# Kernel optimization log

Hardware: AMD Instinct MI355X
Metric: run time of the kernel (lower is better)

## Reference

```python
import jax, jax.numpy as jnp
import numpy as np


def _cosine_alpha_bar(T, s=0.008):
    x = np.linspace(0.0, T, T + 1)
    ac = np.cos((x / T + s) / (1.0 + s) * np.pi / 2.0) ** 2
    ac = ac / ac[0]
    betas = np.clip(1.0 - ac[1:] / ac[:-1], 1e-5, 0.999)
    return jnp.asarray(np.cumprod(1.0 - betas), dtype=jnp.float32)


def setup_inputs():
    B, T, C, D, L, NS = 16, 1024, 16, 256, 4, 1000
    ks = list(jax.random.split(jax.random.key(0), 64))
    def w(i, shape, fan):
        return jax.random.normal(ks[i], shape, dtype=jnp.float32) / np.sqrt(fan)
    half = D // 2
    nf = half // 2
    inp = {}
    inp['x'] = jax.random.normal(ks[0], (B, T, C), dtype=jnp.float32)
    inp['t'] = jax.random.randint(ks[1], (B,), 0, NS, dtype=jnp.int32)
    dt = jax.random.uniform(ks[2], (B, T), minval=5e-4, maxval=2e-3, dtype=jnp.float32)
    inp['timestamps'] = jnp.cumsum(dt, axis=1)
    inp['mask'] = (jax.random.uniform(ks[3], (B, T, C)) > 0.3).astype(jnp.float32)
    inp['noise'] = jax.random.normal(ks[4], (B, T, D), dtype=jnp.float32)
    inp['n_heads'] = 4
    inp['alpha_bar'] = _cosine_alpha_bar(NS)
    inp['W_enc'] = w(5, (2 * C, D), 2 * C); inp['b_enc'] = jnp.zeros((D,), jnp.float32)
    inp['te_freqs'] = jnp.exp(-jnp.arange(half, dtype=jnp.float32) * np.log(10000.0) / half)
    inp['W_temb'] = w(6, (D, D), D); inp['b_temb'] = jnp.zeros((D,), jnp.float32)
    inp['th_a'] = 0.1 * jax.random.normal(ks[7], (half,), dtype=jnp.float32)
    inp['th_b'] = 0.1 * jax.random.normal(ks[8], (half,), dtype=jnp.float32)
    inp['th_freqs'] = (jnp.exp(-jnp.linspace(0.0, np.log(10000.0 / 4.0), nf)) * (2.0 * np.pi / 4.0)).astype(jnp.float32)
    inp['W_film'] = w(9, (D, 2 * D), D); inp['b_film'] = jnp.zeros((2 * D,), jnp.float32)
    inp['gru_Wih'] = w(10, (D, 3 * D), D); inp['gru_Whh'] = w(11, (D, 3 * D), D)
    inp['gru_bih'] = jnp.zeros((3 * D,), jnp.float32); inp['gru_bhh'] = jnp.zeros((3 * D,), jnp.float32)
    inp['ode_W1'] = w(12, (D, D), D); inp['ode_b1'] = jnp.zeros((D,), jnp.float32)
    inp['ode_W2'] = w(13, (D, D), D); inp['ode_b2'] = jnp.zeros((D,), jnp.float32)
    inp['tr_Wqkv'] = w(14, (L, D, 3 * D), D); inp['tr_bqkv'] = jnp.zeros((L, 3 * D), jnp.float32)
    inp['tr_Wo'] = w(15, (L, D, D), D); inp['tr_bo'] = jnp.zeros((L, D), jnp.float32)
    inp['tr_ln1_w'] = jnp.ones((L, D), jnp.float32); inp['tr_ln1_b'] = jnp.zeros((L, D), jnp.float32)
    inp['tr_ln2_w'] = jnp.ones((L, D), jnp.float32); inp['tr_ln2_b'] = jnp.zeros((L, D), jnp.float32)
    inp['tr_W1'] = w(16, (L, D, 4 * D), D); inp['tr_b1'] = jnp.zeros((L, 4 * D), jnp.float32)
    inp['tr_W2'] = w(17, (L, 4 * D, D), 4 * D); inp['tr_b2'] = jnp.zeros((L, D), jnp.float32)
    inp['trn_w'] = jnp.ones((D,), jnp.float32); inp['trn_b'] = jnp.zeros((D,), jnp.float32)
    return inp


def _ln(u, w_, b_):
    m = u.mean(-1, keepdims=True)
    v = u.var(-1, keepdims=True)
    return (u - m) / jnp.sqrt(v + 1e-5) * w_ + b_


def reference(x, t, timestamps, mask, noise, n_heads, alpha_bar, W_enc, b_enc, te_freqs, W_temb, b_temb, th_a, th_b, th_freqs, W_film, b_film, gru_Wih, gru_Whh, gru_bih, gru_bhh, ode_W1, ode_b1, ode_W2, ode_b2, tr_Wqkv, tr_bqkv, tr_Wo, tr_bo, tr_ln1_w, tr_ln1_b, tr_ln2_w, tr_ln2_b, tr_W1, tr_b1, tr_W2, tr_b2, trn_w, trn_b):
    B, T, C = x.shape
    D = W_enc.shape[1]
    hd = D // n_heads
    # latent encode + forward diffusion
    z = jax.nn.relu(jnp.concatenate([x, mask], -1) @ W_enc + b_enc)  # (B,T,D)
    ab = alpha_bar[t][:, None, None]
    h = jnp.sqrt(ab) * z + jnp.sqrt(1.0 - ab) * noise
    # diffusion-step sinusoidal embedding
    targ = t.astype(jnp.float32)[:, None] * te_freqs[None, :]
    te = (jnp.concatenate([jnp.sin(targ), jnp.cos(targ)], -1) @ W_temb + b_temb)[:, None, :]
    # TimeHybridEncoding: odd dims ramp, even dims interleaved sin/cos
    ts = timestamps
    ramp = ts[..., None] * th_a + th_b                       # (B,T,D/2)
    phase = ts[..., None] * th_freqs                         # (B,T,D/4)
    sc = jnp.stack([jnp.sin(phase), jnp.cos(phase)], -1).reshape(B, T, -1)
    tm = jnp.zeros((B, T, D), x.dtype).at[..., 0::2].set(sc).at[..., 1::2].set(ramp)
    gamma, beta = jnp.split(jax.nn.silu(te) @ W_film + b_film, 2, -1)
    tm = (1.0 + gamma) * tm + beta
    h = h + te + tm
    # Jump-ODE encoder: RK4 between events + GRUCell jump, as a scan
    dts = jnp.concatenate([jnp.zeros((B, 1), x.dtype), ts[:, 1:] - ts[:, :-1]], 1)[..., None]  # (B,T,1); dt0=0 -> identity ODE step
    def odef(hh):
        return jnp.tanh(hh @ ode_W1 + ode_b1) @ ode_W2 + ode_b2
    def step(hh, inp):
        xt, dt = inp
        f1 = odef(hh)
        f2 = odef(hh + 0.5 * dt * f1)
        f3 = odef(hh + 0.5 * dt * f2)
        f4 = odef(hh + dt * f3)
        hh = hh + dt / 6.0 * (f1 + 2.0 * f2 + 2.0 * f3 + f4)
        gi = xt @ gru_Wih + gru_bih
        gh = hh @ gru_Whh + gru_bhh
        ir, iz, inn = jnp.split(gi, 3, -1)
        hr, hz, hn = jnp.split(gh, 3, -1)
        r = jax.nn.sigmoid(ir + hr)
        zg = jax.nn.sigmoid(iz + hz)
        n = jnp.tanh(inn + r * hn)
        hh = (1.0 - zg) * n + zg * hh
        return hh, hh
    _, Hs = jax.lax.scan(step, jnp.zeros((B, D), x.dtype), (jnp.swapaxes(h, 0, 1), jnp.swapaxes(dts, 0, 1)))
    Hseq = jnp.swapaxes(Hs, 0, 1)  # (B,T,D)
    # pre-norm causal transformer encoder (eval mode, relu FFN), final LayerNorm
    causal = jnp.triu(jnp.full((T, T), -jnp.inf, dtype=x.dtype), 1)
    Ht = Hseq
    for l in range(tr_Wqkv.shape[0]):
        u = _ln(Ht, tr_ln1_w[l], tr_ln1_b[l])
        q, k, v = jnp.split(u @ tr_Wqkv[l] + tr_bqkv[l], 3, -1)
        q = q.reshape(B, T, n_heads, hd).transpose(0, 2, 1, 3)
        k = k.reshape(B, T, n_heads, hd).transpose(0, 2, 1, 3)
        v = v.reshape(B, T, n_heads, hd).transpose(0, 2, 1, 3)
        att = jax.nn.softmax(jnp.einsum('bhqd,bhkd->bhqk', q, k) / np.sqrt(hd) + causal, axis=-1)
        o = jnp.einsum('bhqk,bhkd->bhqd', att, v).transpose(0, 2, 1, 3).reshape(B, T, D)
        Ht = Ht + o @ tr_Wo[l] + tr_bo[l]
        u2 = _ln(Ht, tr_ln2_w[l], tr_ln2_b[l])
        Ht = Ht + jax.nn.relu(u2 @ tr_W1[l] + tr_b1[l]) @ tr_W2[l] + tr_b2[l]
    Ht = _ln(Ht, trn_w, trn_b)
    return Hseq + Ht
```

## Files before the change

### kernel.cpp

```cpp
#include <hip/hip_runtime.h>

#define Bz  16
#define Tz  1024
#define Cz  16
#define Dz  256
#define NHz 4
#define HDz 64
#define Lz  4
#define MROWS (Bz*Tz)
#define QB  8

__device__ __forceinline__ float sigmoidf_(float x){ return 1.0f/(1.0f+__expf(-x)); }
__device__ __forceinline__ float tanh_(float x){
  float e = __expf(2.f*x);
  return 1.f - 2.f/(e + 1.f);
}

__device__ __forceinline__ float dot2f(uint a, uint b, float c){
  float d;
  asm("v_dot2_f32_f16 %0, %1, %2, %3" : "=v"(d) : "v"(a), "v"(b), "v"(c));
  return d;
}
__device__ __forceinline__ uint f2h2(float a, float b){
  union { _Float16 h[2]; uint u; } r;
  r.h[0] = (_Float16)a; r.h[1] = (_Float16)b;
  return r.u;
}

__device__ __forceinline__ float red8(float a){
  int x = __builtin_amdgcn_update_dpp(0, __float_as_int(a), 0xB1, 0xF, 0xF, true);
  a += __int_as_float(x);
  x = __builtin_amdgcn_update_dpp(0, __float_as_int(a), 0x4E, 0xF, 0xF, true);
  a += __int_as_float(x);
  a += __shfl_xor(a, 4);
  return a;
}

#define BARSYNC() do{ \
  asm volatile("s_waitcnt lgkmcnt(0)" ::: "memory"); \
  __builtin_amdgcn_s_barrier(); \
}while(0)

typedef const __attribute__((address_space(1))) void* as1p;
typedef __attribute__((address_space(3))) void* as3p;

__global__ __launch_bounds__(256) void k_prep(
    const float* __restrict__ W1, const float* __restrict__ W2, const float* __restrict__ Whh,
    const float* __restrict__ bih, const float* __restrict__ bhh,
    uint* __restrict__ W1L, uint* __restrict__ W2L, uint* __restrict__ WhL,
    float* __restrict__ biasC)
{
  int m = blockIdx.x*256 + threadIdx.x;
  if (m < 65536){
    const float* W = (m < 32768) ? W1 : W2;
    uint* out = (m < 32768) ? W1L : W2L;
    int mm = m & 32767;
    int q = mm >> 2, cc = mm & 3;
    int i = q >> 9, l = q & 511;
    int j4 = l >> 3, ks = l & 7;
    int kp = ks*16 + i;
    int c = j4*4 + cc;
    out[mm] = f2h2(W[(2*kp)*256 + c], W[(2*kp+1)*256 + c]);
  } else if (m < 65536 + 98304){
    int mm = m - 65536;
    int g = mm >> 15;
    int r = mm & 32767;
    int q = r >> 2, cc = r & 3;
    int i = q >> 9, l = q & 511;
    int j4 = l >> 3, ks = l & 7;
    int kp = ks*16 + i;
    int c = j4*4 + cc;
    WhL[mm] = f2h2(Whh[(2*kp)*768 + g*256 + c], Whh[(2*kp+1)*768 + g*256 + c]);
  } else if (m < 65536 + 98304 + 768){
    int c = m - (65536 + 98304);
    biasC[c] = bih[c] + ((c < 512) ? bhh[c] : 0.f);
  }
}

__global__ __launch_bounds__(256) void k_batch_emb(
    const int* __restrict__ t, const float* __restrict__ te_freqs,
    const float* __restrict__ W_temb, const float* __restrict__ b_temb,
    const float* __restrict__ W_film, const float* __restrict__ b_film,
    float* __restrict__ te_out, float* __restrict__ gamma_out, float* __restrict__ beta_out)
{
  int b = blockIdx.x; int j = threadIdx.x;
  __shared__ float s[256];
  __shared__ float ste[256];
  float tf = (float)t[b];
  if (j < 128){
    float targ = tf * te_freqs[j];
    s[j]     = __sinf(targ);
    s[j+128] = __cosf(targ);
  }
  __syncthreads();
  float a0=0,a1=0,a2=0,a3=0;
  #pragma unroll 8
  for (int k=0;k<256;k+=4){
    a0 = fmaf(s[k+0], W_temb[(k+0)*256+j], a0);
    a1 = fmaf(s[k+1], W_temb[(k+1)*256+j], a1);
    a2 = fmaf(s[k+2], W_temb[(k+2)*256+j], a2);
    a3 = fmaf(s[k+3], W_temb[(k+3)*256+j], a3);
  }
  float te = (a0+a1)+(a2+a3) + b_temb[j];
  te_out[b*256+j] = te;
  ste[j] = te * sigmoidf_(te);
  __syncthreads();
  float g0=0,g1=0,h0=0,h1=0;
  #pragma unroll 8
  for (int k=0;k<256;k+=2){
    float v0 = ste[k+0], v1 = ste[k+1];
    g0 = fmaf(v0, W_film[(k+0)*512+j],     g0);
    g1 = fmaf(v1, W_film[(k+1)*512+j],     g1);
    h0 = fmaf(v0, W_film[(k+0)*512+256+j], h0);
    h1 = fmaf(v1, W_film[(k+1)*512+256+j], h1);
  }
  gamma_out[b*256+j] = g0+g1 + b_film[j];
  beta_out [b*256+j] = h0+h1 + b_film[256+j];
}

__global__ __launch_bounds__(256) void k_encode(
    const float* __restrict__ x, const float* __restrict__ mask, const float* __restrict__ noise,
    const int* __restrict__ t, const float* __restrict__ alpha_bar, const float* __restrict__ ts,
    const float* __restrict__ W_enc, const float* __restrict__ b_enc,
    const float* __restrict__ th_a, const float* __restrict__ th_b, const float* __restrict__ th_freqs,
    const float* __restrict__ te, const float* __restrict__ gamma, const float* __restrict__ beta,
    float* __restrict__ H0)
{
  int bt = blockIdx.x; int b = bt >> 10;
  int j = threadIdx.x;
  __shared__ float in[32];
  if (j < 16)      in[j] = x[bt*16 + j];
  else if (j < 32) in[j] = mask[bt*16 + (j-16)];
  __syncthreads();
  float acc = 0.f;
  #pragma unroll
  for (int k=0;k<32;k++) acc = fmaf(in[k], W_enc[k*256+j], acc);
  float z = fmaxf(acc + b_enc[j], 0.f);
  float ab = alpha_bar[t[b]];
  float h = sqrtf(ab)*z + sqrtf(1.f-ab)*noise[(size_t)bt*256 + j];
  float tsv = ts[bt];
  float tm;
  if (j & 1){
    int i = (j-1) >> 1;
    tm = fmaf(tsv, th_a[i], th_b[i]);
  } else {
    int m = j >> 2;
    float ph = tsv * th_freqs[m];
    tm = ((j & 3) == 0) ? __sinf(ph) : __cosf(ph);
  }
  tm = fmaf(1.f + gamma[b*256+j], tm, beta[b*256+j]);
  H0[(size_t)bt*256 + j] = h + te[b*256+j] + tm;
}

template<bool RELU, bool RES>
__global__ __launch_bounds__(256) void k_gemm(
    const float* __restrict__ A, const float* __restrict__ W,
    const float* __restrict__ bias, const float* __restrict__ Rp,
    float* __restrict__ Cp, int M, int N, int K)
{
  __shared__ float As[16][68];
  __shared__ float Bs[16][64];
  int bn = blockIdx.x * 64, bm = blockIdx.y * 64;
  int tid = threadIdx.x;
  int tx = tid & 15, ty = tid >> 4;
  float acc[4][4] = {};
  for (int k0=0; k0<K; k0+=16){
    #pragma unroll
    for (int i=0;i<4;i++){
      int idx = tid + i*256;
      int m = idx >> 4, kk = idx & 15;
      As[kk][m] = A[(size_t)(bm+m)*K + k0+kk];
    }
    #pragma unroll
    for (int i=0;i<4;i++){
      int idx = tid + i*256;
      int kk = idx >> 6, n = idx & 63;
      Bs[kk][n] = W[(size_t)(k0+kk)*N + bn+n];
    }
    __syncthreads();
    #pragma unroll
    for (int kk=0;kk<16;kk++){
      float a0=As[kk][ty*4+0], a1=As[kk][ty*4+1], a2=As[kk][ty*4+2], a3=As[kk][ty*4+3];
      float b0=Bs[kk][tx*4+0], b1=Bs[kk][tx*4+1], b2=Bs[kk][tx*4+2], b3=Bs[kk][tx*4+3];
      acc[0][0]=fmaf(a0,b0,acc[0][0]); acc[0][1]=fmaf(a0,b1,acc[0][1]); acc[0][2]=fmaf(a0,b2,acc[0][2]); acc[0][3]=fmaf(a0,b3,acc[0][3]);
      acc[1][0]=fmaf(a1,b0,acc[1][0]); acc[1][1]=fmaf(a1,b1,acc[1][1]); acc[1][2]=fmaf(a1,b2,acc[1][2]); acc[1][3]=fmaf(a1,b3,acc[1][3]);
      acc[2][0]=fmaf(a2,b0,acc[2][0]); acc[2][1]=fmaf(a2,b1,acc[2][1]); acc[2][2]=fmaf(a2,b2,acc[2][2]); acc[2][3]=fmaf(a2,b3,acc[2][3]);
      acc[3][0]=fmaf(a3,b0,acc[3][0]); acc[3][1]=fmaf(a3,b1,acc[3][1]); acc[3][2]=fmaf(a3,b2,acc[3][2]); acc[3][3]=fmaf(a3,b3,acc[3][3]);
    }
    __syncthreads();
  }
  #pragma unroll
  for (int i=0;i<4;i++){
    int row = bm + ty*4 + i;
    #pragma unroll
    for (int jj=0;jj<4;jj++){
      int col = bn + tx*4 + jj;
      float v = acc[i][jj] + bias[col];
      if (RELU) v = fmaxf(v, 0.f);
      if (RES)  v += Rp[(size_t)row*N + col];
      Cp[(size_t)row*N + col] = v;
    }
  }
}

#define W1_BYTES   131072
#define RING_OFF   131072
#define RING_BYTES 24576
#define V2_OFF     (RING_OFF + RING_BYTES)
#define SCAN_LDS_BYTES (V2_OFF + 1280)

#define DOT4V(WV, VW) { uint4 _w = (WV); \
  a0 = dot2f(_w.x, VW, a0); a1 = dot2f(_w.y, VW, a1); \
  a2 = dot2f(_w.z, VW, a2); a3 = dot2f(_w.w, VW, a3); }

#define MV16L(VB) { \
  uint4 q0=(VB)[ks5+0], q1=(VB)[ks5+1], q2=(VB)[ks5+2], q3=(VB)[ks5+3]; \
  DOT4V(w1s[0*512+tid], q0.x)  DOT4V(w1s[1*512+tid], q0.y)  DOT4V(w1s[2*512+tid], q0.z)  DOT4V(w1s[3*512+tid], q0.w)  \
  DOT4V(w1s[4*512+tid], q1.x)  DOT4V(w1s[5*512+tid], q1.y)  DOT4V(w1s[6*512+tid], q1.z)  DOT4V(w1s[7*512+tid], q1.w)  \
  DOT4V(w1s[8*512+tid], q2.x)  DOT4V(w1s[9*512+tid], q2.y)  DOT4V(w1s[10*512+tid], q2.z) DOT4V(w1s[11*512+tid], q2.w) \
  DOT4V(w1s[12*512+tid], q3.x) DOT4V(w1s[13*512+tid], q3.y) DOT4V(w1s[14*512+tid], q3.z) DOT4V(w1s[15*512+tid], q3.w) }

#define MV16R(W, VB) { \
  uint4 q0=(VB)[ks5+0], q1=(VB)[ks5+1], q2=(VB)[ks5+2], q3=(VB)[ks5+3]; \
  DOT4V(W[0], q0.x)  DOT4V(W[1], q0.y)  DOT4V(W[2], q0.z)  DOT4V(W[3], q0.w)  \
  DOT4V(W[4], q1.x)  DOT4V(W[5], q1.y)  DOT4V(W[6], q1.z)  DOT4V(W[7], q1.w)  \
  DOT4V(W[8], q2.x)  DOT4V(W[9], q2.y)  DOT4V(W[10], q2.z) DOT4V(W[11], q2.w) \
  DOT4V(W[12], q3.x) DOT4V(W[13], q3.y) DOT4V(W[14], q3.z) DOT4V(W[15], q3.w) }

#define RING_STEP(S, N, G0,G1,G2,G3) { \
  asm volatile("s_waitcnt vmcnt(" #N ")" ::: "memory"); \
  uint4 wv = *(const uint4*)(ringRd + (((S)%3)<<10) + lane16); \
  G0 = dot2f(wv.x, vw[(S)&15], G0); G1 = dot2f(wv.y, vw[(S)&15], G1); \
  G2 = dot2f(wv.z, vw[(S)&15], G2); G3 = dot2f(wv.w, vw[(S)&15], G3); \
  __builtin_amdgcn_global_load_lds((as1p)(WhL4 + ((((S)+3)%48)<<9) + tid), \
                                   (as3p)(ringRd + (((S)%3)<<10)), 16, 0, 0); \
}

__global__ __launch_bounds__(512) void k_scan(
    const uint* __restrict__ W1Lg, const uint* __restrict__ W2Lg, const uint* __restrict__ WhLg,
    const float* __restrict__ GI, const float* __restrict__ ts,
    const float* __restrict__ b1, const float* __restrict__ b2,
    const float* __restrict__ bhh, float* __restrict__ Hseq)
{
  extern __shared__ __align__(16) char smem[];
  uint4* w1s = (uint4*)smem;
  uint*  v2  = (uint*)(smem + V2_OFF);
  const int b = blockIdx.x, tid = threadIdx.x;
  const int j4 = tid >> 3, ks = tid & 7;
  const int ks5 = ks*5;
  char* ringRd = smem + RING_OFF + (tid >> 6)*3072;
  const int lane16 = (tid & 63) << 4;
  const uint4* W1L4 = (const uint4*)W1Lg;
  const uint4* W2L4 = (const uint4*)W2Lg;
  const uint4* WhL4 = (const uint4*)WhLg;
  #pragma unroll
  for (int i=0;i<16;i++) w1s[i*512+tid] = W1L4[i*512+tid];
  uint4 w2r[16];
  #pragma unroll
  for (int i=0;i<16;i++) w2r[i] = W2L4[i*512 + tid];
  if (tid < 320) v2[tid] = 0u;
  const float4 b1v  = ((const float4*)b1)[j4];
  const float4 b2v  = ((const float4*)b2)[j4];
  const float4 bhnv = ((const float4*)bhh)[128 + j4];
  const float* tsb = ts + b*Tz;
  const float* gib = GI + (size_t)b*Tz*768;
  float* hsq = Hseq + (size_t)b*Tz*256;
  const int wdw = 2*j4;
  const int wslot = (wdw >> 4)*20 + (wdw & 15);
  float4 h = {0.f,0.f,0.f,0.f};
  int cur = 0;
  float tprev = 0.f;
  __syncthreads();

  #pragma unroll
  for (int s=0;s<3;s++)
    __builtin_amdgcn_global_load_lds((as1p)(WhL4 + (s<<9) + tid),
                                     (as3p)(ringRd + (s<<10)), 16, 0, 0);
  float4 gi_r = *(const float4*)(gib + 0*768       + j4*4);
  float4 gi_z = *(const float4*)(gib + 0*768 + 256 + j4*4);
  float4 gi_n = *(const float4*)(gib + 0*768 + 512 + j4*4);

  for (int tt=0; tt<Tz; ++tt){
    float tcur = tsb[tt];
    float dt = tcur - tprev; if (tt == 0) dt = 0.f;
    tprev = tcur;
    uint* bufA = v2 + (cur ? 160 : 0);
    uint* bufB = v2 + (cur ? 0 : 160);
    const uint4* vbA = (const uint4*)bufA;
    const uint4* vbB = (const uint4*)bufB;

    {
      float a0=0,a1=0,a2=0,a3=0;
      MV16L(vbA);
      a0=red8(a0); a1=red8(a1); a2=red8(a2); a3=red8(a3);
      float u0 = tanh_(a0+b1v.x), u1 = tanh_(a1+b1v.y);
      float u2 = tanh_(a2+b1v.z), u3 = tanh_(a3+b1v.w);
      if (ks == 0){
        uint2 pk; pk.x = f2h2(u0,u1); pk.y = f2h2(u2,u3);
        *(uint2*)(bufB + wslot) = pk;
      }
    }
    BARSYNC();
    float4 hn;
    {
      float a0=0,a1=0,a2=0,a3=0;
      MV16R(w2r, vbB);
      a0=red8(a0); a1=red8(a1); a2=red8(a2); a3=red8(a3);
      hn.x = fmaf(dt, a0+b2v.x, h.x);
      hn.y = fmaf(dt, a1+b2v.y, h.y);
      hn.z = fmaf(dt, a2+b2v.z, h.z);
      hn.w = fmaf(dt, a3+b2v.w, h.w);
      if (ks == 0){
        uint2 pk; pk.x = f2h2(hn.x,hn.y); pk.y = f2h2(hn.z,hn.w);
        *(uint2*)(bufA + wslot) = pk;
      }
    }
    BARSYNC();
    {
      uint4 q0=vbA[ks5+0], q1=vbA[ks5+1], q2=vbA[ks5+2], q3=vbA[ks5+3];
      uint vw[16] = {q0.x,q0.y,q0.z,q0.w, q1.x,q1.y,q1.z,q1.w,
                     q2.x,q2.y,q2.z,q2.w, q3.x,q3.y,q3.z,q3.w};
      float r0=0,r1=0,r2=0,r3=0, z0=0,z1=0,z2=0,z3=0, n0=0,n1=0,n2=0,n3=0;
      RING_STEP(0,3, r0,r1,r2,r3)  RING_STEP(1,3, r0,r1,r2,r3)
      RING_STEP(2,3, r0,r1,r2,r3)  RING_STEP(3,2, r0,r1,r2,r3)
      RING_STEP(4,2, r0,r1,r2,r3)  RING_STEP(5,2, r0,r1,r2,r3)
      RING_STEP(6,2, r0,r1,r2,r3)  RING_STEP(7,2, r0,r1,r2,r3)
      RING_STEP(8,2, r0,r1,r2,r3)  RING_STEP(9,2, r0,r1,r2,r3)
      RING_STEP(10,2, r0,r1,r2,r3) RING_STEP(11,2, r0,r1,r2,r3)
      RING_STEP(12,2, r0,r1,r2,r3) RING_STEP(13,2, r0,r1,r2,r3)
      RING_STEP(14,2, r0,r1,r2,r3) RING_STEP(15,2, r0,r1,r2,r3)
      RING_STEP(16,2, z0,z1,z2,z3) RING_STEP(17,2, z0,z1,z2,z3)
      RING_STEP(18,2, z0,z1,z2,z3) RING_STEP(19,2, z0,z1,z2,z3)
      RING_STEP(20,2, z0,z1,z2,z3) RING_STEP(21,2, z0,z1,z2,z3)
      RING_STEP(22,2, z0,z1,z2,z3) RING_STEP(23,2, z0,z1,z2,z3)
      RING_STEP(24,2, z0,z1,z2,z3) RING_STEP(25,2, z0,z1,z2,z3)
      RING_STEP(26,2, z0,z1,z2,z3) RING_STEP(27,2, z0,z1,z2,z3)
      RING_STEP(28,2, z0,z1,z2,z3) RING_STEP(29,2, z0,z1,z2,z3)
      RING_STEP(30,2, z0,z1,z2,z3) RING_STEP(31,2, z0,z1,z2,z3)
      RING_STEP(32,2, n0,n1,n2,n3) RING_STEP(33,2, n0,n1,n2,n3)
      RING_STEP(34,2, n0,n1,n2,n3) RING_STEP(35,2, n0,n1,n2,n3)
      RING_STEP(36,2, n0,n1,n2,n3) RING_STEP(37,2, n0,n1,n2,n3)
      RING_STEP(38,2, n0,n1,n2,n3) RING_STEP(39,2, n0,n1,n2,n3)
      RING_STEP(40,2, n0,n1,n2,n3) RING_STEP(41,2, n0,n1,n2,n3)
      RING_STEP(42,2, n0,n1,n2,n3) RING_STEP(43,2, n0,n1,n2,n3)
      RING_STEP(44,2, n0,n1,n2,n3)
      int ttn = (tt+1 < Tz) ? tt+1 : Tz-1;
      float4 ngi_r = *(const float4*)(gib + ttn*768       + j4*4);
      float4 ngi_z = *(const float4*)(gib + ttn*768 + 256 + j4*4);
      float4 ngi_n = *(const float4*)(gib + ttn*768 + 512 + j4*4);
      RING_STEP(45,2, n0,n1,n2,n3) RING_STEP(46,2, n0,n1,n2,n3)
      RING_STEP(47,2, n0,n1,n2,n3)
      r0=red8(r0); r1=red8(r1); r2=red8(r2); r3=red8(r3);
      z0=red8(z0); z1=red8(z1); z2=red8(z2); z3=red8(z3);
      n0=red8(n0); n1=red8(n1); n2=red8(n2); n3=red8(n3);
      float gr0 = sigmoidf_(gi_r.x + r0);
      float gr1 = sigmoidf_(gi_r.y + r1);
      float gr2 = sigmoidf_(gi_r.z + r2);
      float gr3 = sigmoidf_(gi_r.w + r3);
      float gz0 = sigmoidf_(gi_z.x + z0);
      float gz1 = sigmoidf_(gi_z.y + z1);
      float gz2 = sigmoidf_(gi_z.z + z2);
      float gz3 = sigmoidf_(gi_z.w + z3);
      float gn0 = tanh_(gi_n.x + gr0*(n0 + bhnv.x));
      float gn1 = tanh_(gi_n.y + gr1*(n1 + bhnv.y));
      float gn2 = tanh_(gi_n.z + gr2*(n2 + bhnv.z));
      float gn3 = tanh_(gi_n.w + gr3*(n3 + bhnv.w));
      h.x = fmaf(gz0, hn.x - gn0, gn0);
      h.y = fmaf(gz1, hn.y - gn1, gn1);
      h.z = fmaf(gz2, hn.z - gn2, gn2);
      h.w = fmaf(gz3, hn.w - gn3, gn3);
      gi_r = ngi_r; gi_z = ngi_z; gi_n = ngi_n;
      if (ks == 0){
        uint2 pk; pk.x = f2h2(h.x,h.y); pk.y = f2h2(h.z,h.w);
        *(uint2*)(bufB + wslot) = pk;
        *(float4*)(hsq + tt*256 + j4*4) = h;
      }
    }
    cur ^= 1;
    BARSYNC();
  }
}

__global__ __launch_bounds__(256) void k_attn(const float* __restrict__ QKV, float* __restrict__ O)
{
  int qb = blockIdx.x & (Tz/QB - 1);
  int bh = blockIdx.x / (Tz/QB);
  int b = bh >> 2, h = bh & 3;
  __shared__ uint Q2[QB][32];
  __shared__ float S[QB][Tz];
  __shared__ __align__(16) char kvbuf[64*68*4];
  __shared__ float rs[QB];
  uint  (*K2)[33] = (uint(*)[33])kvbuf;
  float (*Vs)[68] = (float(*)[68])kvbuf;
  int tid = threadIdx.x;
  const float* base = QKV + (size_t)b*Tz*768;
  for (int i = tid; i < QB*16; i += 256){
    int q = i >> 4, c = i & 15;
    const float4 v = *(const float4*)&base[(size_t)(qb*QB+q)*768 + h*64 + c*4];
    Q2[q][c*2]   = f2h2(v.x*0.125f, v.y*0.125f);
    Q2[q][c*2+1] = f2h2(v.z*0.125f, v.w*0.125f);
  }
  __syncthreads();
  int kmax = qb*QB + QB;
  int nkt = (kmax + 63) >> 6;
  int q = tid >> 5, i0 = tid & 31;
  int qg = qb*QB + q;
  for (int kt=0; kt<nkt; ++kt){
    for (int i=tid; i<64*16; i+=256){
      int r=i>>4, c=i&15;
      const float4 v = *(const float4*)&base[(size_t)(kt*64+r)*768 + 256 + h*64 + c*4];
      K2[r][c*2]   = f2h2(v.x, v.y);
      K2[r][c*2+1] = f2h2(v.z, v.w);
    }
    __syncthreads();
    float a0=0.f, a1=0.f;
    #pragma unroll 8
    for (int dp=0; dp<32; ++dp){
      uint qv = Q2[q][dp];
      a0 = dot2f(K2[i0][dp],    qv, a0);
      a1 = dot2f(K2[i0+32][dp], qv, a1);
    }
    int k0g = kt*64 + i0, k1g = k0g + 32;
    S[q][kt*64+i0]    = (k0g <= qg) ? a0 : -1e30f;
    S[q][kt*64+i0+32] = (k1g <= qg) ? a1 : -1e30f;
    __syncthreads();
  }
  int NK = nkt*64;
  float m = -1e30f;
  for (int kk=i0; kk<NK; kk+=32) m = fmaxf(m, S[q][kk]);
  #pragma unroll
  for (int o=16;o;o>>=1) m = fmaxf(m, __shfl_xor(m, o, 32));
  float sum = 0.f;
  for (int kk=i0; kk<NK; kk+=32){
    float p = __expf(S[q][kk] - m);
    S[q][kk] = p;
    sum += p;
  }
  #pragma unroll
  for (int o=16;o;o>>=1) sum += __shfl_xor(sum, o, 32);
  if (i0 == 0) rs[q] = 1.f/sum;
  int dq = tid & 15;
  int ks = (tid >> 4) & 1;
  float o0=0,o1=0,o2=0,o3=0;
  for (int kt=0; kt<nkt; ++kt){
    __syncthreads();
    for (int i=tid; i<64*16; i+=256){
      int r=i>>4, c=i&15;
      const float4 v = *(const float4*)&base[(size_t)(kt*64+r)*768 + 512 + h*64 + c*4];
      *(float4*)&Vs[r][c*4] = v;
    }
    __syncthreads();
    int kbase = kt*64;
    #pragma unroll 8
    for (int kk=ks; kk<64; kk+=2){
      float p = S[q][kbase+kk];
      const float4 vv = *(const float4*)&Vs[kk][dq*4];
      o0=fmaf(p,vv.x,o0); o1=fmaf(p,vv.y,o1); o2=fmaf(p,vv.z,o2); o3=fmaf(p,vv.w,o3);
    }
  }
  o0 += __shfl_xor(o0, 16); o1 += __shfl_xor(o1, 16);
  o2 += __shfl_xor(o2, 16); o3 += __shfl_xor(o3, 16);
  if (!(tid & 16)){
    float r = rs[q];
    size_t orow = ((size_t)b*Tz + qg)*256 + h*64 + dq*4;
    float4 ov = {o0*r, o1*r, o2*r, o3*r};
    *(float4*)&O[orow] = ov;
  }
}

template<bool FINAL>
__global__ __launch_bounds__(256) void k_ln(
    const float* __restrict__ in, const float* __restrict__ w, const float* __restrict__ bgain,
    const float* __restrict__ addv, float* __restrict__ out)
{
  int row  = blockIdx.x*4 + (threadIdx.x >> 6);
  int lane = threadIdx.x & 63;
  const float4 xv = ((const float4*)(in + (size_t)row*256))[lane];
  float s = xv.x + xv.y + xv.z + xv.w;
  #pragma unroll
  for (int o=32;o;o>>=1) s += __shfl_xor(s, o, 64);
  float mean = s * (1.f/256.f);
  float dx=xv.x-mean, dy=xv.y-mean, dz=xv.z-mean, dw=xv.w-mean;
  float qv = dx*dx + dy*dy + dz*dz + dw*dw;
  #pragma unroll
  for (int o=32;o;o>>=1) qv += __shfl_xor(qv, o, 64);
  float rstd = 1.f/sqrtf(qv*(1.f/256.f) + 1e-5f);
  const float4 wv = ((const float4*)w)[lane];
  const float4 bv = ((const float4*)bgain)[lane];
  float4 ov;
  ov.x = dx*rstd*wv.x + bv.x;
  ov.y = dy*rstd*wv.y + bv.y;
  ov.z = dz*rstd*wv.z + bv.z;
  ov.w = dw*rstd*wv.w + bv.w;
  if (FINAL){
    const float4 av = ((const float4*)(addv + (size_t)row*256))[lane];
    ov.x += av.x; ov.y += av.y; ov.z += av.z; ov.w += av.w;
  }
  ((float4*)(out + (size_t)row*256))[lane] = ov;
}

extern "C" void kernel_launch(void* const* d_in, const int* in_sizes, int n_in,
                              void* d_out, int out_size, void* d_ws, size_t ws_size,
                              hipStream_t stream)
{
  const float* x         = (const float*)d_in[0];
  const int*   t         = (const int*)  d_in[1];
  const float* ts        = (const float*)d_in[2];
  const float* mask      = (const float*)d_in[3];
  const float* noise     = (const float*)d_in[4];
  const float* alpha_bar = (const float*)d_in[6];
  const float* W_enc     = (const float*)d_in[7];
  const float* b_enc     = (const float*)d_in[8];
  const float* te_freqs  = (const float*)d_in[9];
  const float* W_temb    = (const float*)d_in[10];
  const float* b_temb    = (const float*)d_in[11];
  const float* th_a      = (const float*)d_in[12];
  const float* th_b      = (const float*)d_in[13];
  const float* th_freqs  = (const float*)d_in[14];
  const float* W_film    = (const float*)d_in[15];
  const float* b_film    = (const float*)d_in[16];
  const float* gru_Wih   = (const float*)d_in[17];
  const float* gru_Whh   = (const float*)d_in[18];
  const float* gru_bih   = (const float*)d_in[19];
  const float* gru_bhh   = (const float*)d_in[20];
  const float* ode_W1    = (const float*)d_in[21];
  const float* ode_b1    = (const float*)d_in[22];
  const float* ode_W2    = (const float*)d_in[23];
  const float* ode_b2    = (const float*)d_in[24];
  const float* tr_Wqkv   = (const float*)d_in[25];
  const float* tr_bqkv   = (const float*)d_in[26];
  const float* tr_Wo     = (const float*)d_in[27];
  const float* tr_bo     = (const float*)d_in[28];
  const float* tr_ln1_w  = (const float*)d_in[29];
  const float* tr_ln1_b  = (const float*)d_in[30];
  const float* tr_ln2_w  = (const float*)d_in[31];
  const float* tr_ln2_b  = (const float*)d_in[32];
  const float* tr_W1     = (const float*)d_in[33];
  const float* tr_b1     = (const float*)d_in[34];
  const float* tr_W2     = (const float*)d_in[35];
  const float* tr_b2     = (const float*)d_in[36];
  const float* trn_w     = (const float*)d_in[37];
  const float* trn_b     = (const float*)d_in[38];

  float* w = (float*)d_ws;
  float* te    = w;
  float* gamma = w + 4096;
  float* beta  = w + 8192;
  float* R1    = w + 12288;
  float* H0    = R1;
  float* GI    = R1 + 4*1024*1024;
  float* QKVb  = R1;
  float* F1    = R1;
  float* Hseq  = R1   + 16*1024*1024;
  float* Ht    = Hseq + 4*1024*1024;
  float* U     = Ht   + 4*1024*1024;
  float* O     = U    + 4*1024*1024;
  uint*  W1L   = (uint*)(O + 4*1024*1024);
  uint*  W2L   = W1L + 32768;
  uint*  WhL   = W2L + 32768;
  float* biasC = (float*)(WhL + 98304);

  k_prep<<<643, 256, 0, stream>>>(ode_W1, ode_W2, gru_Whh, gru_bih, gru_bhh,
                                  W1L, W2L, WhL, biasC);
  k_batch_emb<<<Bz, 256, 0, stream>>>(t, te_freqs, W_temb, b_temb, W_film, b_film, te, gamma, beta);
  k_encode<<<MROWS, 256, 0, stream>>>(x, mask, noise, t, alpha_bar, ts, W_enc, b_enc,
                                      th_a, th_b, th_freqs, te, gamma, beta, H0);
  k_gemm<false,false><<<dim3(768/64, MROWS/64), 256, 0, stream>>>(H0, gru_Wih, biasC, nullptr, GI, MROWS, 768, 256);

  hipFuncSetAttribute((const void*)k_scan, hipFuncAttributeMaxDynamicSharedMemorySize, SCAN_LDS_BYTES);
  k_scan<<<Bz, 512, SCAN_LDS_BYTES, stream>>>(W1L, W2L, WhL, GI, ts, ode_b1, ode_b2, gru_bhh, Hseq);

  for (int l=0; l<Lz; ++l){
    const float* Hin = (l == 0) ? Hseq : Ht;
    k_ln<false><<<MROWS/4, 256, 0, stream>>>(Hin, tr_ln1_w + l*256, tr_ln1_b + l*256, nullptr, U);
    k_gemm<false,false><<<dim3(768/64, MROWS/64), 256, 0, stream>>>(U, tr_Wqkv + (size_t)l*256*768, tr_bqkv + l*768, nullptr, QKVb, MROWS, 768, 256);
    k_attn<<<Bz*NHz*(Tz/QB), 256, 0, stream>>>(QKVb, O);
    k_gemm<false,true><<<dim3(256/64, MROWS/64), 256, 0, stream>>>(O, tr_Wo + (size_t)l*256*256, tr_bo + l*256, Hin, Ht, MROWS, 256, 256);
    k_ln<false><<<MROWS/4, 256, 0, stream>>>(Ht, tr_ln2_w + l*256, tr_ln2_b + l*256, nullptr, U);
    k_gemm<true,false><<<dim3(1024/64, MROWS/64), 256, 0, stream>>>(U, tr_W1 + (size_t)l*256*1024, tr_b1 + l*1024, nullptr, F1, MROWS, 1024, 256);
    k_gemm<false,true><<<dim3(256/64, MROWS/64), 256, 0, stream>>>(F1, tr_W2 + (size_t)l*1024*256, tr_b2 + l*256, Ht, Ht, MROWS, 256, 1024);
  }

  k_ln<true><<<MROWS/4, 256, 0, stream>>>(Ht, trn_w, trn_b, Hseq, (float*)d_out);
}
```

Measured before the change: 11.71 ms.

## Stream W1 and Whh through a deeper unified per-wave LDS ring

Stops keeping W1 resident in LDS. W1 (16 panels) and the GRU hidden weights (48 panels) now stream through one 16-slot per-wave LDS ring as a 64-panel cycle, with 12 panels in flight and consumption in groups of four. The ring was previously 3 slots deep and covered only the Whh weights, so the intent is to hide global/L2 latency and free LDS. The cost is re-reading W1 from L2 every step, and the vmcnt accounting across the next-step GI loads is tighter and could go wrong.

```diff
diff --git a/kernel.cpp b/kernel.cpp
--- a/kernel.cpp
+++ b/kernel.cpp
@@ -203,38 +203,35 @@
   }
 }
 
-#define W1_BYTES   131072
-#define RING_OFF   131072
-#define RING_BYTES 24576
-#define V2_OFF     (RING_OFF + RING_BYTES)
+#define RING_WAVE_BYTES 16384
+#define V2_OFF 131072
 #define SCAN_LDS_BYTES (V2_OFF + 1280)
+
+#define WRP(p)  ((p) < 64 ? (p) : (p)-64)
+#define SRCP(p) ((p) < 16 ? (W1L4 + (p)*512 + tid) : (WhL4 + ((p)-16)*512 + tid))
+#define ISSUE1(pu) __builtin_amdgcn_global_load_lds((as1p)SRCP(WRP(pu)), \
+                     (as3p)(ringRd + (((pu)&15)<<10)), 16, 0, 0);
+
+#define GRP(g, V, A0,A1,A2,A3) { \
+  asm volatile("s_waitcnt vmcnt(8)" ::: "memory"); \
+  uint4 wv0 = *(const uint4*)(ringRd + (((4*(g)+0)&15)<<10) + lane16); \
+  uint4 wv1 = *(const uint4*)(ringRd + (((4*(g)+1)&15)<<10) + lane16); \
+  uint4 wv2 = *(const uint4*)(ringRd + (((4*(g)+2)&15)<<10) + lane16); \
+  uint4 wv3 = *(const uint4*)(ringRd + (((4*(g)+3)&15)<<10) + lane16); \
+  A0=dot2f(wv0.x,(V)[(4*(g)+0)&15],A0); A1=dot2f(wv0.y,(V)[(4*(g)+0)&15],A1); \
+  A2=dot2f(wv0.z,(V)[(4*(g)+0)&15],A2); A3=dot2f(wv0.w,(V)[(4*(g)+0)&15],A3); \
+  A0=dot2f(wv1.x,(V)[(4*(g)+1)&15],A0); A1=dot2f(wv1.y,(V)[(4*(g)+1)&15],A1); \
+  A2=dot2f(wv1.z,(V)[(4*(g)+1)&15],A2); A3=dot2f(wv1.w,(V)[(4*(g)+1)&15],A3); \
+  A0=dot2f(wv2.x,(V)[(4*(g)+2)&15],A0); A1=dot2f(wv2.y,(V)[(4*(g)+2)&15],A1); \
+  A2=dot2f(wv2.z,(V)[(4*(g)+2)&15],A2); A3=dot2f(wv2.w,(V)[(4*(g)+2)&15],A3); \
+  A0=dot2f(wv3.x,(V)[(4*(g)+3)&15],A0); A1=dot2f(wv3.y,(V)[(4*(g)+3)&15],A1); \
+  A2=dot2f(wv3.z,(V)[(4*(g)+3)&15],A2); A3=dot2f(wv3.w,(V)[(4*(g)+3)&15],A3); \
+  ISSUE1(4*(g)+12) ISSUE1(4*(g)+13) ISSUE1(4*(g)+14) ISSUE1(4*(g)+15) \
+}
 
 #define DOT4V(WV, VW) { uint4 _w = (WV); \
   a0 = dot2f(_w.x, VW, a0); a1 = dot2f(_w.y, VW, a1); \
   a2 = dot2f(_w.z, VW, a2); a3 = dot2f(_w.w, VW, a3); }
-
-#define MV16L(VB) { \
-  uint4 q0=(VB)[ks5+0], q1=(VB)[ks5+1], q2=(VB)[ks5+2], q3=(VB)[ks5+3]; \
-  DOT4V(w1s[0*512+tid], q0.x)  DOT4V(w1s[1*512+tid], q0.y)  DOT4V(w1s[2*512+tid], q0.z)  DOT4V(w1s[3*512+tid], q0.w)  \
-  DOT4V(w1s[4*512+tid], q1.x)  DOT4V(w1s[5*512+tid], q1.y)  DOT4V(w1s[6*512+tid], q1.z)  DOT4V(w1s[7*512+tid], q1.w)  \
-  DOT4V(w1s[8*512+tid], q2.x)  DOT4V(w1s[9*512+tid], q2.y)  DOT4V(w1s[10*512+tid], q2.z) DOT4V(w1s[11*512+tid], q2.w) \
-  DOT4V(w1s[12*512+tid], q3.x) DOT4V(w1s[13*512+tid], q3.y) DOT4V(w1s[14*512+tid], q3.z) DOT4V(w1s[15*512+tid], q3.w) }
-
-#define MV16R(W, VB) { \
-  uint4 q0=(VB)[ks5+0], q1=(VB)[ks5+1], q2=(VB)[ks5+2], q3=(VB)[ks5+3]; \
-  DOT4V(W[0], q0.x)  DOT4V(W[1], q0.y)  DOT4V(W[2], q0.z)  DOT4V(W[3], q0.w)  \
-  DOT4V(W[4], q1.x)  DOT4V(W[5], q1.y)  DOT4V(W[6], q1.z)  DOT4V(W[7], q1.w)  \
-  DOT4V(W[8], q2.x)  DOT4V(W[9], q2.y)  DOT4V(W[10], q2.z) DOT4V(W[11], q2.w) \
-  DOT4V(W[12], q3.x) DOT4V(W[13], q3.y) DOT4V(W[14], q3.z) DOT4V(W[15], q3.w) }
-
-#define RING_STEP(S, N, G0,G1,G2,G3) { \
-  asm volatile("s_waitcnt vmcnt(" #N ")" ::: "memory"); \
-  uint4 wv = *(const uint4*)(ringRd + (((S)%3)<<10) + lane16); \
-  G0 = dot2f(wv.x, vw[(S)&15], G0); G1 = dot2f(wv.y, vw[(S)&15], G1); \
-  G2 = dot2f(wv.z, vw[(S)&15], G2); G3 = dot2f(wv.w, vw[(S)&15], G3); \
-  __builtin_amdgcn_global_load_lds((as1p)(WhL4 + ((((S)+3)%48)<<9) + tid), \
-                                   (as3p)(ringRd + (((S)%3)<<10)), 16, 0, 0); \
-}
 
 __global__ __launch_bounds__(512) void k_scan(
     const uint* __restrict__ W1Lg, const uint* __restrict__ W2Lg, const uint* __restrict__ WhLg,
@@ -243,18 +240,15 @@
     const float* __restrict__ bhh, float* __restrict__ Hseq)
 {
   extern __shared__ __align__(16) char smem[];
-  uint4* w1s = (uint4*)smem;
-  uint*  v2  = (uint*)(smem + V2_OFF);
-  const int b = blockIdx.x, tid = threadIdx.x;
+  uint* v2 = (uint*)(smem + V2_OFF);
+  const int tid = threadIdx.x, b = blockIdx.x;
   const int j4 = tid >> 3, ks = tid & 7;
   const int ks5 = ks*5;
-  char* ringRd = smem + RING_OFF + (tid >> 6)*3072;
+  char* ringRd = smem + (tid >> 6)*RING_WAVE_BYTES;
   const int lane16 = (tid & 63) << 4;
   const uint4* W1L4 = (const uint4*)W1Lg;
   const uint4* W2L4 = (const uint4*)W2Lg;
   const uint4* WhL4 = (const uint4*)WhLg;
-  #pragma unroll
-  for (int i=0;i<16;i++) w1s[i*512+tid] = W1L4[i*512+tid];
   uint4 w2r[16];
   #pragma unroll
   for (int i=0;i<16;i++) w2r[i] = W2L4[i*512 + tid];
@@ -273,9 +267,9 @@
   __syncthreads();
 
   #pragma unroll
-  for (int s=0;s<3;s++)
-    __builtin_amdgcn_global_load_lds((as1p)(WhL4 + (s<<9) + tid),
-                                     (as3p)(ringRd + (s<<10)), 16, 0, 0);
+  for (int p=0;p<12;p++)
+    __builtin_amdgcn_global_load_lds((as1p)(W1L4 + p*512 + tid),
+                                     (as3p)(ringRd + (p<<10)), 16, 0, 0);
   float4 gi_r = *(const float4*)(gib + 0*768       + j4*4);
   float4 gi_z = *(const float4*)(gib + 0*768 + 256 + j4*4);
   float4 gi_n = *(const float4*)(gib + 0*768 + 512 + j4*4);
@@ -290,8 +284,14 @@
     const uint4* vbB = (const uint4*)bufB;
 
     {
+      uint4 q0=vbA[ks5+0], q1=vbA[ks5+1], q2=vbA[ks5+2], q3=vbA[ks5+3];
+      uint vh[16] = {q0.x,q0.y,q0.z,q0.w, q1.x,q1.y,q1.z,q1.w,
+                     q2.x,q2.y,q2.z,q2.w, q3.x,q3.y,q3.z,q3.w};
       float a0=0,a1=0,a2=0,a3=0;
-      MV16L(vbA);
+      GRP(0, vh, a0,a1,a2,a3)
+      GRP(1, vh, a0,a1,a2,a3)
+      GRP(2, vh, a0,a1,a2,a3)
+      GRP(3, vh, a0,a1,a2,a3)
       a0=red8(a0); a1=red8(a1); a2=red8(a2); a3=red8(a3);
       float u0 = tanh_(a0+b1v.x), u1 = tanh_(a1+b1v.y);
       float u2 = tanh_(a2+b1v.z), u3 = tanh_(a3+b1v.w);
@@ -303,8 +303,12 @@
     BARSYNC();
     float4 hn;
     {
+      uint4 p0=vbB[ks5+0], p1=vbB[ks5+1], p2=vbB[ks5+2], p3=vbB[ks5+3];
+      uint vu[16] = {p0.x,p0.y,p0.z,p0.w, p1.x,p1.y,p1.z,p1.w,
+                     p2.x,p2.y,p2.z,p2.w, p3.x,p3.y,p3.z,p3.w};
       float a0=0,a1=0,a2=0,a3=0;
-      MV16R(w2r, vbB);
+      #pragma unroll
+      for (int i=0;i<16;i++){ DOT4V(w2r[i], vu[i]); }
       a0=red8(a0); a1=red8(a1); a2=red8(a2); a3=red8(a3);
       hn.x = fmaf(dt, a0+b2v.x, h.x);
       hn.y = fmaf(dt, a1+b2v.y, h.y);
@@ -317,39 +321,26 @@
     }
     BARSYNC();
     {
-      uint4 q0=vbA[ks5+0], q1=vbA[ks5+1], q2=vbA[ks5+2], q3=vbA[ks5+3];
-      uint vw[16] = {q0.x,q0.y,q0.z,q0.w, q1.x,q1.y,q1.z,q1.w,
-                     q2.x,q2.y,q2.z,q2.w, q3.x,q3.y,q3.z,q3.w};
+      uint4 g0=vbA[ks5+0], g1=vbA[ks5+1], g2=vbA[ks5+2], g3=vbA[ks5+3];
+      uint vn[16] = {g0.x,g0.y,g0.z,g0.w, g1.x,g1.y,g1.z,g1.w,
+                     g2.x,g2.y,g2.z,g2.w, g3.x,g3.y,g3.z,g3.w};
       float r0=0,r1=0,r2=0,r3=0, z0=0,z1=0,z2=0,z3=0, n0=0,n1=0,n2=0,n3=0;
-      RING_STEP(0,3, r0,r1,r2,r3)  RING_STEP(1,3, r0,r1,r2,r3)
-      RING_STEP(2,3, r0,r1,r2,r3)  RING_STEP(3,2, r0,r1,r2,r3)
-      RING_STEP(4,2, r0,r1,r2,r3)  RING_STEP(5,2, r0,r1,r2,r3)
-      RING_STEP(6,2, r0,r1,r2,r3)  RING_STEP(7,2, r0,r1,r2,r3)
-      RING_STEP(8,2, r0,r1,r2,r3)  RING_STEP(9,2, r0,r1,r2,r3)
-      RING_STEP(10,2, r0,r1,r2,r3) RING_STEP(11,2, r0,r1,r2,r3)
-      RING_STEP(12,2, r0,r1,r2,r3) RING_STEP(13,2, r0,r1,r2,r3)
-      RING_STEP(14,2, r0,r1,r2,r3) RING_STEP(15,2, r0,r1,r2,r3)
-      RING_STEP(16,2, z0,z1,z2,z3) RING_STEP(17,2, z0,z1,z2,z3)
-      RING_STEP(18,2, z0,z1,z2,z3) RING_STEP(19,2, z0,z1,z2,z3)
-      RING_STEP(20,2, z0,z1,z2,z3) RING_STEP(21,2, z0,z1,z2,z3)
-      RING_STEP(22,2, z0,z1,z2,z3) RING_STEP(23,2, z0,z1,z2,z3)
-      RING_STEP(24,2, z0,z1,z2,z3) RING_STEP(25,2, z0,z1,z2,z3)
-      RING_STEP(26,2, z0,z1,z2,z3) RING_STEP(27,2, z0,z1,z2,z3)
-      RING_STEP(28,2, z0,z1,z2,z3) RING_STEP(29,2, z0,z1,z2,z3)
-      RING_STEP(30,2, z0,z1,z2,z3) RING_STEP(31,2, z0,z1,z2,z3)
-      RING_STEP(32,2, n0,n1,n2,n3) RING_STEP(33,2, n0,n1,n2,n3)
-      RING_STEP(34,2, n0,n1,n2,n3) RING_STEP(35,2, n0,n1,n2,n3)
-      RING_STEP(36,2, n0,n1,n2,n3) RING_STEP(37,2, n0,n1,n2,n3)
-      RING_STEP(38,2, n0,n1,n2,n3) RING_STEP(39,2, n0,n1,n2,n3)
-      RING_STEP(40,2, n0,n1,n2,n3) RING_STEP(41,2, n0,n1,n2,n3)
-      RING_STEP(42,2, n0,n1,n2,n3) RING_STEP(43,2, n0,n1,n2,n3)
-      RING_STEP(44,2, n0,n1,n2,n3)
+      GRP(4,  vn, r0,r1,r2,r3)
+      GRP(5,  vn, r0,r1,r2,r3)
+      GRP(6,  vn, r0,r1,r2,r3)
+      GRP(7,  vn, r0,r1,r2,r3)
+      GRP(8,  vn, z0,z1,z2,z3)
+      GRP(9,  vn, z0,z1,z2,z3)
+      GRP(10, vn, z0,z1,z2,z3)
+      GRP(11, vn, z0,z1,z2,z3)
+      GRP(12, vn, n0,n1,n2,n3)
+      GRP(13, vn, n0,n1,n2,n3)
       int ttn = (tt+1 < Tz) ? tt+1 : Tz-1;
       float4 ngi_r = *(const float4*)(gib + ttn*768       + j4*4);
       float4 ngi_z = *(const float4*)(gib + ttn*768 + 256 + j4*4);
       float4 ngi_n = *(const float4*)(gib + ttn*768 + 512 + j4*4);
-      RING_STEP(45,2, n0,n1,n2,n3) RING_STEP(46,2, n0,n1,n2,n3)
-      RING_STEP(47,2, n0,n1,n2,n3)
+      GRP(14, vn, n0,n1,n2,n3)
+      GRP(15, vn, n0,n1,n2,n3)
       r0=red8(r0); r1=red8(r1); r2=red8(r2); r3=red8(r3);
       z0=red8(z0); z1=red8(z1); z2=red8(z2); z3=red8(z3);
       n0=red8(n0); n1=red8(n1); n2=red8(n2); n3=red8(n3);
```

After: 12.29 ms. 4.9% more time.

## Switch dense GEMMs to fp16 MFMA with prepacked half-precision weights

Applied to the files above, without the earlier changes.

Replaces the scalar fp32 64x64-tile GEMM with a 128x128-tile kernel that issues 16x16x32 fp16 MFMA instructions, converting activations to fp16 in LDS. A new pack kernel converts the weights into k-blocked fp16 uint4 layout in d_out scratch before use, which the final LN later overwrites. This aims to move the transformer and GRU input projections onto the matrix cores. It trades precision for speed, and larger tiles give fewer blocks for the N=256 GEMMs.

```diff
diff --git a/kernel.cpp b/kernel.cpp
--- a/kernel.cpp
+++ b/kernel.cpp
@@ -9,6 +9,9 @@
 #define Lz  4
 #define MROWS (Bz*Tz)
 #define QB  8
+
+typedef _Float16 half8_t __attribute__((ext_vector_type(8)));
+typedef float    f32x4_t __attribute__((ext_vector_type(4)));
 
 __device__ __forceinline__ float sigmoidf_(float x){ return 1.0f/(1.0f+__expf(-x)); }
 __device__ __forceinline__ float tanh_(float x){
@@ -77,6 +80,21 @@
   }
 }
 
+__global__ __launch_bounds__(256) void k_packw(
+    const float* __restrict__ W, uint4* __restrict__ Wp, int N, int total)
+{
+  int idx = blockIdx.x*256 + threadIdx.x;
+  if (idx >= total) return;
+  int col = idx % N, kr = idx / N;
+  size_t kb = (size_t)kr*8;
+  uint4 o;
+  o.x = f2h2(W[(kb+0)*N+col], W[(kb+1)*N+col]);
+  o.y = f2h2(W[(kb+2)*N+col], W[(kb+3)*N+col]);
+  o.z = f2h2(W[(kb+4)*N+col], W[(kb+5)*N+col]);
+  o.w = f2h2(W[(kb+6)*N+col], W[(kb+7)*N+col]);
+  Wp[idx] = o;
+}
+
 __global__ __launch_bounds__(256) void k_batch_emb(
     const int* __restrict__ t, const float* __restrict__ te_freqs,
     const float* __restrict__ W_temb, const float* __restrict__ b_temb,
@@ -154,51 +172,62 @@
 
 template<bool RELU, bool RES>
 __global__ __launch_bounds__(256) void k_gemm(
-    const float* __restrict__ A, const float* __restrict__ W,
+    const float* __restrict__ A, const uint4* __restrict__ Wp,
     const float* __restrict__ bias, const float* __restrict__ Rp,
     float* __restrict__ Cp, int M, int N, int K)
 {
-  __shared__ float As[16][68];
-  __shared__ float Bs[16][64];
-  int bn = blockIdx.x * 64, bm = blockIdx.y * 64;
-  int tid = threadIdx.x;
-  int tx = tid & 15, ty = tid >> 4;
-  float acc[4][4] = {};
-  for (int k0=0; k0<K; k0+=16){
+  __shared__ _Float16 Asl[128][40];
+  __shared__ uint4    Bsl[4][128];
+  const int bn = blockIdx.x*128, bm = blockIdx.y*128;
+  const int tid = threadIdx.x;
+  const int lane = tid & 63, w = tid >> 6;
+  const int wr = (w >> 1)*64, wc = (w & 1)*64;
+  const int l15 = lane & 15, l4 = lane >> 4;
+  f32x4_t acc[4][4] = {};
+  for (int k0 = 0; k0 < K; k0 += 32){
     #pragma unroll
     for (int i=0;i<4;i++){
       int idx = tid + i*256;
-      int m = idx >> 4, kk = idx & 15;
-      As[kk][m] = A[(size_t)(bm+m)*K + k0+kk];
-    }
+      int row = idx >> 3, q = idx & 7;
+      const float4 a4 = *(const float4*)&A[(size_t)(bm+row)*K + k0 + q*4];
+      uint2 pk; pk.x = f2h2(a4.x, a4.y); pk.y = f2h2(a4.z, a4.w);
+      *(uint2*)&Asl[row][q*4] = pk;
+    }
+    const uint4* wsrc = Wp + (size_t)(k0 >> 5)*4*N + bn;
     #pragma unroll
-    for (int i=0;i<4;i++){
+    for (int i=0;i<2;i++){
       int idx = tid + i*256;
-      int kk = idx >> 6, n = idx & 63;
-      Bs[kk][n] = W[(size_t)(k0+kk)*N + bn+n];
+      int kb = idx >> 7, col = idx & 127;
+      Bsl[kb][col] = wsrc[(size_t)kb*N + col];
     }
     __syncthreads();
+    half8_t bf[4];
     #pragma unroll
-    for (int kk=0;kk<16;kk++){
-      float a0=As[kk][ty*4+0], a1=As[kk][ty*4+1], a2=As[kk][ty*4+2], a3=As[kk][ty*4+3];
-      float b0=Bs[kk][tx*4+0], b1=Bs[kk][tx*4+1], b2=Bs[kk][tx*4+2], b3=Bs[kk][tx*4+3];
-      acc[0][0]=fmaf(a0,b0,acc[0][0]); acc[0][1]=fmaf(a0,b1,acc[0][1]); acc[0][2]=fmaf(a0,b2,acc[0][2]); acc[0][3]=fmaf(a0,b3,acc[0][3]);
-      acc[1][0]=fmaf(a1,b0,acc[1][0]); acc[1][1]=fmaf(a1,b1,acc[1][1]); acc[1][2]=fmaf(a1,b2,acc[1][2]); acc[1][3]=fmaf(a1,b3,acc[1][3]);
-      acc[2][0]=fmaf(a2,b0,acc[2][0]); acc[2][1]=fmaf(a2,b1,acc[2][1]); acc[2][2]=fmaf(a2,b2,acc[2][2]); acc[2][3]=fmaf(a2,b3,acc[2][3]);
-      acc[3][0]=fmaf(a3,b0,acc[3][0]); acc[3][1]=fmaf(a3,b1,acc[3][1]); acc[3][2]=fmaf(a3,b2,acc[3][2]); acc[3][3]=fmaf(a3,b3,acc[3][3]);
+    for (int tn=0; tn<4; tn++)
+      bf[tn] = *(const half8_t*)&Bsl[l4][wc + tn*16 + l15];
+    #pragma unroll
+    for (int tm=0; tm<4; tm++){
+      half8_t af = *(const half8_t*)&Asl[wr + tm*16 + l15][l4*8];
+      #pragma unroll
+      for (int tn=0; tn<4; tn++)
+        acc[tm][tn] = __builtin_amdgcn_mfma_f32_16x16x32_f16(af, bf[tn], acc[tm][tn], 0, 0, 0);
     }
     __syncthreads();
   }
   #pragma unroll
-  for (int i=0;i<4;i++){
-    int row = bm + ty*4 + i;
+  for (int tm=0;tm<4;tm++){
     #pragma unroll
-    for (int jj=0;jj<4;jj++){
-      int col = bn + tx*4 + jj;
-      float v = acc[i][jj] + bias[col];
-      if (RELU) v = fmaxf(v, 0.f);
-      if (RES)  v += Rp[(size_t)row*N + col];
-      Cp[(size_t)row*N + col] = v;
+    for (int tn=0;tn<4;tn++){
+      int col = bn + wc + tn*16 + l15;
+      float bcol = bias[col];
+      #pragma unroll
+      for (int r=0;r<4;r++){
+        int row = bm + wr + tm*16 + l4*4 + r;
+        float v = acc[tm][tn][r] + bcol;
+        if (RELU) v = fmaxf(v, 0.f);
+        if (RES)  v += Rp[(size_t)row*N + col];
+        Cp[(size_t)row*N + col] = v;
+      }
     }
   }
 }
@@ -560,12 +589,23 @@
   uint*  WhL   = W2L + 32768;
   float* biasC = (float*)(WhL + 98304);
 
+  uint4* WihP  = (uint4*)d_out;
+  uint4* WqkvP = WihP  + 24576;
+  uint4* WoP   = WqkvP + 98304;
+  uint4* W1P   = WoP   + 32768;
+  uint4* W2P   = W1P   + 131072;
+
   k_prep<<<643, 256, 0, stream>>>(ode_W1, ode_W2, gru_Whh, gru_bih, gru_bhh,
                                   W1L, W2L, WhL, biasC);
+  k_packw<<<96,  256, 0, stream>>>(gru_Wih, WihP, 768, 24576);
+  k_packw<<<384, 256, 0, stream>>>(tr_Wqkv, WqkvP, 768, 98304);
+  k_packw<<<128, 256, 0, stream>>>(tr_Wo,   WoP,   256, 32768);
+  k_packw<<<512, 256, 0, stream>>>(tr_W1,   W1P,  1024, 131072);
+  k_packw<<<512, 256, 0, stream>>>(tr_W2,   W2P,   256, 131072);
   k_batch_emb<<<Bz, 256, 0, stream>>>(t, te_freqs, W_temb, b_temb, W_film, b_film, te, gamma, beta);
   k_encode<<<MROWS, 256, 0, stream>>>(x, mask, noise, t, alpha_bar, ts, W_enc, b_enc,
                                       th_a, th_b, th_freqs, te, gamma, beta, H0);
-  k_gemm<false,false><<<dim3(768/64, MROWS/64), 256, 0, stream>>>(H0, gru_Wih, biasC, nullptr, GI, MROWS, 768, 256);
+  k_gemm<false,false><<<dim3(768/128, MROWS/128), 256, 0, stream>>>(H0, WihP, biasC, nullptr, GI, MROWS, 768, 256);
 
   hipFuncSetAttribute((const void*)k_scan, hipFuncAttributeMaxDynamicSharedMemorySize, SCAN_LDS_BYTES);
   k_scan<<<Bz, 512, SCAN_LDS_BYTES, stream>>>(W1L, W2L, WhL, GI, ts, ode_b1, ode_b2, gru_bhh, Hseq);
@@ -573,12 +613,12 @@
   for (int l=0; l<Lz; ++l){
     const float* Hin = (l == 0) ? Hseq : Ht;
     k_ln<false><<<MROWS/4, 256, 0, stream>>>(Hin, tr_ln1_w + l*256, tr_ln1_b + l*256, nullptr, U);
-    k_gemm<false,false><<<dim3(768/64, MROWS/64), 256, 0, stream>>>(U, tr_Wqkv + (size_t)l*256*768, tr_bqkv + l*768, nullptr, QKVb, MROWS, 768, 256);
+    k_gemm<false,false><<<dim3(768/128, MROWS/128), 256, 0, stream>>>(U, WqkvP + (size_t)l*24576, tr_bqkv + l*768, nullptr, QKVb, MROWS, 768, 256);
     k_attn<<<Bz*NHz*(Tz/QB), 256, 0, stream>>>(QKVb, O);
-    k_gemm<false,true><<<dim3(256/64, MROWS/64), 256, 0, stream>>>(O, tr_Wo + (size_t)l*256*256, tr_bo + l*256, Hin, Ht, MROWS, 256, 256);
+    k_gemm<false,true><<<dim3(256/128, MROWS/128), 256, 0, stream>>>(O, WoP + (size_t)l*8192, tr_bo + l*256, Hin, Ht, MROWS, 256, 256);
     k_ln<false><<<MROWS/4, 256, 0, stream>>>(Ht, tr_ln2_w + l*256, tr_ln2_b + l*256, nullptr, U);
-    k_gemm<true,false><<<dim3(1024/64, MROWS/64), 256, 0, stream>>>(U, tr_W1 + (size_t)l*256*1024, tr_b1 + l*1024, nullptr, F1, MROWS, 1024, 256);
-    k_gemm<false,true><<<dim3(256/64, MROWS/64), 256, 0, stream>>>(F1, tr_W2 + (size_t)l*1024*256, tr_b2 + l*256, Ht, Ht, MROWS, 256, 1024);
+    k_gemm<true,false><<<dim3(1024/128, MROWS/128), 256, 0, stream>>>(U, W1P + (size_t)l*32768, tr_b1 + l*1024, nullptr, F1, MROWS, 1024, 256);
+    k_gemm<false,true><<<dim3(256/128, MROWS/128), 256, 0, stream>>>(F1, W2P + (size_t)l*32768, tr_b2 + l*256, Ht, Ht, MROWS, 256, 1024);
   }
 
   k_ln<true><<<MROWS/4, 256, 0, stream>>>(Ht, trn_w, trn_b, Hseq, (float*)d_out);
```

Result: faster. 10.44 ms (median of 2 runs) (-10.9%).
